# Optimization experiments

Hardware: AMD Instinct MI355X
Metric: run time of the kernel (lower is better)

## Reference

```python
import jax, jax.numpy as jnp
import numpy as np

N_NODES = 50000
N_EDGES = 800000
IN_DIM = 768
HIDDEN = 256
N_CLASSES = 10
N_GRAPHS = 128


def setup_inputs() -> dict:
    key = jax.random.key(0)
    ks = jax.random.split(key, 10)
    emb = jax.random.normal(ks[0], (N_NODES, IN_DIM), dtype=jnp.float32)
    edge_index = jax.random.randint(ks[1], (2, N_EDGES), 0, N_NODES, dtype=jnp.int32)
    batch = jnp.sort(jax.random.randint(ks[2], (N_NODES,), 0, N_GRAPHS, dtype=jnp.int32))
    # GCNConv weights (glorot-ish scale) and biases
    W1 = jax.random.normal(ks[3], (IN_DIM, HIDDEN), dtype=jnp.float32) / np.sqrt(IN_DIM)
    b1 = jnp.zeros((HIDDEN,), dtype=jnp.float32)
    W2 = jax.random.normal(ks[4], (HIDDEN, HIDDEN), dtype=jnp.float32) / np.sqrt(HIDDEN)
    b2 = jnp.zeros((HIDDEN,), dtype=jnp.float32)
    Wfc = jax.random.normal(ks[5], (HIDDEN, N_CLASSES), dtype=jnp.float32) / np.sqrt(HIDDEN)
    bfc = jnp.zeros((N_CLASSES,), dtype=jnp.float32)
    return {"emb": emb, "edge_index": edge_index, "batch": batch,
            "W1": W1, "b1": b1, "W2": W2, "b2": b2, "Wfc": Wfc, "bfc": bfc}


def _gcn_conv(x, src, dst, W, b, n_nodes):
    # PyG GCNConv: x' = D^{-1/2} (A + I) D^{-1/2} X W + b, self-loops included
    h = x @ W                                   # [N, H] dense GEMM
    deg = jax.ops.segment_sum(jnp.ones_like(dst, dtype=h.dtype), dst,
                              num_segments=n_nodes)
    dinv = jnp.where(deg > 0, jax.lax.rsqrt(deg), 0.0)
    norm = dinv[src] * dinv[dst]                # [E+N]
    msgs = h[src] * norm[:, None]               # gather [E+N, H]
    out = jax.ops.segment_sum(msgs, dst, num_segments=n_nodes)  # scatter-add
    return out + b


def reference(emb, edge_index, batch, W1, b1, W2, b2, Wfc, bfc):
    n_nodes = emb.shape[0]
    loops = jnp.arange(n_nodes, dtype=edge_index.dtype)
    src = jnp.concatenate([edge_index[0], loops])  # add self-loops
    dst = jnp.concatenate([edge_index[1], loops])

    x = jax.nn.relu(_gcn_conv(emb, src, dst, W1, b1, n_nodes))
    # F.dropout(p=0.3) is a no-op in eval mode (training=False)
    x = _gcn_conv(x, src, dst, W2, b2, n_nodes)

    # global_mean_pool over graph ids
    sums = jax.ops.segment_sum(x, batch, num_segments=N_GRAPHS)
    cnts = jax.ops.segment_sum(jnp.ones((n_nodes,), dtype=x.dtype), batch,
                               num_segments=N_GRAPHS)
    pooled = sums / jnp.maximum(cnts, 1.0)[:, None]  # [G, H]
    return pooled @ Wfc + bfc                        # [G, C]
```

## Files before the change

### kernel.cpp

```cpp
#include <hip/hip_runtime.h>

#define N_NODES 50000
#define N_EDGES 800000
#define IN_DIM 768
#define HIDDEN 256
#define N_CLASSES 10
#define N_GRAPHS 128

typedef __attribute__((ext_vector_type(8))) short bf16x8;
typedef __attribute__((ext_vector_type(4))) float f32x4;
typedef __attribute__((ext_vector_type(8))) unsigned short u16x8;

__device__ __forceinline__ float bf2f(unsigned short u) {
    union { unsigned int i; float f; } c; c.i = ((unsigned int)u) << 16; return c.f;
}
__device__ __forceinline__ unsigned short f2bf(float f) {
    unsigned int x = __float_as_uint(f);
    return (unsigned short)((x + 0x7fffu + ((x >> 16) & 1u)) >> 16);
}

__device__ __forceinline__ void gload16(const void* g, void* l) {
    __builtin_amdgcn_global_load_lds((const __attribute__((address_space(1))) void*)g,
                                     (__attribute__((address_space(3))) void*)l, 16, 0, 0);
}

__global__ void zero_int(int* p, int n) {
    int i = blockIdx.x * blockDim.x + threadIdx.x;
    if (i < n) p[i] = 0;
}

__global__ void zero_f32(float* p, int n) {
    int i = blockIdx.x * blockDim.x + threadIdx.x;
    if (i < n) p[i] = 0.f;
}

__global__ void hist_dst(const int* __restrict__ dst, int* __restrict__ cnt) {
    int e = blockIdx.x * blockDim.x + threadIdx.x;
    if (e < N_EDGES) atomicAdd(&cnt[dst[e]], 1);
}

__global__ __launch_bounds__(1024) void scan_kernel(const int* __restrict__ cnt,
                                                    int* __restrict__ rowstart,
                                                    int* __restrict__ cursor,
                                                    float* __restrict__ dinv) {
    __shared__ int wsum[16];
    __shared__ int chunk_carry;
    const int tid = threadIdx.x, lane = tid & 63, wid = tid >> 6;
    if (tid == 0) chunk_carry = 0;
    __syncthreads();
    for (int base = 0; base < N_NODES; base += 1024) {
        int i = base + tid;
        int v = (i < N_NODES) ? cnt[i] : 0;
        if (i < N_NODES) dinv[i] = rsqrtf(1.0f + (float)v);
        int s = v;
#pragma unroll
        for (int d = 1; d < 64; d <<= 1) { int t = __shfl_up(s, d); if (lane >= d) s += t; }
        if (lane == 63) wsum[wid] = s;
        __syncthreads();
        if (tid < 16) {
            int ww = wsum[tid];
#pragma unroll
            for (int d = 1; d < 16; d <<= 1) { int t = __shfl_up(ww, d); if (tid >= d) ww += t; }
            wsum[tid] = ww;
        }
        __syncthreads();
        int wpre = (wid == 0) ? 0 : wsum[wid - 1];
        int excl = chunk_carry + wpre + s - v;
        if (i < N_NODES) { rowstart[i] = excl; cursor[i] = excl; }
        int total = wsum[15];
        __syncthreads();
        if (tid == 0) chunk_carry += total;
        __syncthreads();
    }
    if (threadIdx.x == 0) rowstart[N_NODES] = chunk_carry;
}

__global__ void scatter_edges(const int* __restrict__ src, const int* __restrict__ dst,
                              int* __restrict__ cursor, int* __restrict__ col) {
    int e = blockIdx.x * blockDim.x + threadIdx.x;
    if (e >= N_EDGES) return;
    int d = dst[e];
    int pos = atomicAdd(&cursor[d], 1);
    col[pos] = src[e];
}

__global__ __launch_bounds__(256) void transpose_w_bf16(const float* __restrict__ W,
                                                        unsigned short* __restrict__ WT, int K) {
    __shared__ float t[32][33];
    int tx = threadIdx.x & 31, ty = threadIdx.x >> 5;
    int k0 = blockIdx.x * 32, n0 = blockIdx.y * 32;
#pragma unroll
    for (int i = 0; i < 4; ++i) {
        int k = k0 + ty + i * 8;
        t[ty + i * 8][tx] = W[(size_t)k * 256 + n0 + tx];
    }
    __syncthreads();
#pragma unroll
    for (int i = 0; i < 4; ++i) {
        int n = n0 + ty + i * 8;
        WT[(size_t)n * K + k0 + tx] = f2bf(t[tx][ty + i * 8]);
    }
}

template <int K, bool CVT>
__global__ __launch_bounds__(256, 4) void gemm_mfma(const void* __restrict__ Av,
                                                    const unsigned short* __restrict__ BT,
                                                    unsigned short* __restrict__ C, int M) {
    __shared__ uint4 sm[2304];
    uint4* As = sm;
    uint4* Bs = sm + 256;
    const int tid = threadIdx.x;
    const int lane = tid & 63, w = tid >> 6;
    const int lr = lane & 15, kg = lane >> 4;
    const int bm = blockIdx.x * 32;

    f32x4 acc[2][4] = {};

    for (int k0 = 0; k0 < K; k0 += 64) {
        if constexpr (CVT) {
            const float* Af = (const float*)Av;
            int r = tid >> 3, g = tid & 7;
            int gs = g ^ (r & 7);
            int rg = bm + r; rg = rg < M ? rg : M - 1;
            const float* p = &Af[(size_t)rg * K + k0 + gs * 8];
            float4 u = *(const float4*)p;
            float4 v = *(const float4*)(p + 4);
            u16x8 o;
            o[0] = f2bf(u.x); o[1] = f2bf(u.y); o[2] = f2bf(u.z); o[3] = f2bf(u.w);
            o[4] = f2bf(v.x); o[5] = f2bf(v.y); o[6] = f2bf(v.z); o[7] = f2bf(v.w);
            *(u16x8*)&As[r * 8 + g] = o;
        } else {
            const unsigned short* Ab = (const unsigned short*)Av;
            int glin = w * 64 + lane;
            int r = glin >> 3, g = glin & 7;
            int gs = g ^ (r & 7);
            int rg = bm + r; rg = rg < M ? rg : M - 1;
            gload16(&Ab[(size_t)rg * K + k0 + gs * 8], &As[w * 64]);
        }
#pragma unroll
        for (int i = 0; i < 8; ++i) {
            int glin = w * 512 + i * 64 + lane;
            int n = glin >> 3, g = glin & 7;
            int gs = g ^ (n & 7);
            gload16(&BT[(size_t)n * K + k0 + gs * 8], &Bs[w * 512 + i * 64]);
        }
        __syncthreads();

#pragma unroll
        for (int h = 0; h < 2; ++h) {
            int r0 = lr, r1 = 16 + lr;
            bf16x8 a0 = *(const bf16x8*)&As[r0 * 8 + ((4 * h + kg) ^ (r0 & 7))];
            bf16x8 a1 = *(const bf16x8*)&As[r1 * 8 + ((4 * h + kg) ^ (r1 & 7))];
#pragma unroll
            for (int f = 0; f < 4; ++f) {
                int nr = 64 * w + 16 * f + lr;
                bf16x8 bf = *(const bf16x8*)&Bs[nr * 8 + ((4 * h + kg) ^ (nr & 7))];
                acc[0][f] = __builtin_amdgcn_mfma_f32_16x16x32_bf16(bf, a0, acc[0][f], 0, 0, 0);
                acc[1][f] = __builtin_amdgcn_mfma_f32_16x16x32_bf16(bf, a1, acc[1][f], 0, 0, 0);
            }
        }
        __syncthreads();
    }
#pragma unroll
    for (int m = 0; m < 2; ++m) {
        int orow = bm + 16 * m + lr;
        if (orow < M) {
#pragma unroll
            for (int f = 0; f < 4; ++f) {
                ushort4 o = make_ushort4(f2bf(acc[m][f][0]), f2bf(acc[m][f][1]),
                                         f2bf(acc[m][f][2]), f2bf(acc[m][f][3]));
                *(ushort4*)&C[(size_t)orow * 256 + 64 * w + 16 * f + 4 * kg] = o;
            }
        }
    }
}

template <bool RELU, bool OUTBF>
__global__ __launch_bounds__(256) void agg_csr(const unsigned short* __restrict__ h,
                                               const float* __restrict__ dinv,
                                               const int* __restrict__ rowstart,
                                               const int* __restrict__ col,
                                               const float* __restrict__ bias,
                                               void* __restrict__ outv) {
    int node = (blockIdx.x * 256 + threadIdx.x) >> 6;
    if (node >= N_NODES) return;
    const int lane = threadIdx.x & 63;
    const int half = lane >> 5, sl = lane & 31;

    float dd = dinv[node];
    float acc[8] = {};

    {
        u16x8 hv = *(const u16x8*)&h[(size_t)node * 256 + sl * 8];
        float wgt = half ? 0.f : dd * dd;
#pragma unroll
        for (int i = 0; i < 8; ++i) acc[i] += bf2f(hv[i]) * wgt;
    }

    int j0 = rowstart[node], jend = rowstart[node + 1];
    for (int j = j0; j < jend; j += 2) {
        int sidx = j + half;
        bool p = sidx < jend;
        int s = p ? col[sidx] : node;
        float nrm = p ? dinv[s] * dd : 0.f;
        u16x8 v = *(const u16x8*)&h[(size_t)s * 256 + sl * 8];
#pragma unroll
        for (int i = 0; i < 8; ++i) acc[i] += bf2f(v[i]) * nrm;
    }

#pragma unroll
    for (int i = 0; i < 8; ++i) acc[i] += __shfl_xor(acc[i], 32);

    if (half == 0) {
        float4 b0 = *(const float4*)&bias[sl * 8];
        float4 b1 = *(const float4*)&bias[sl * 8 + 4];
        acc[0] += b0.x; acc[1] += b0.y; acc[2] += b0.z; acc[3] += b0.w;
        acc[4] += b1.x; acc[5] += b1.y; acc[6] += b1.z; acc[7] += b1.w;
        if (RELU) {
#pragma unroll
            for (int i = 0; i < 8; ++i) acc[i] = fmaxf(acc[i], 0.f);
        }
        if (OUTBF) {
            u16x8 o;
#pragma unroll
            for (int i = 0; i < 8; ++i) o[i] = f2bf(acc[i]);
            *(u16x8*)((unsigned short*)outv + (size_t)node * 256 + sl * 8) = o;
        } else {
            float* ob = (float*)outv + (size_t)node * 256 + sl * 8;
            *(float4*)ob = make_float4(acc[0], acc[1], acc[2], acc[3]);
            *(float4*)(ob + 4) = make_float4(acc[4], acc[5], acc[6], acc[7]);
        }
    }
}

#define POOL_CHUNK 49
__global__ __launch_bounds__(256) void pool_partial(const float* __restrict__ x,
                                                    const int* __restrict__ batch,
                                                    float* __restrict__ gsum) {
    int lo = blockIdx.x * POOL_CHUNK;
    if (lo >= N_NODES) return;
    int hi = lo + POOL_CHUNK; if (hi > N_NODES) hi = N_NODES;
    int c = threadIdx.x;
    int g = batch[lo];
    float acc = 0.f;
    for (int n = lo; n < hi; ++n) {
        int gn = batch[n];
        if (gn != g) { atomicAdd(&gsum[g * 256 + c], acc); acc = 0.f; g = gn; }
        acc += x[(size_t)n * 256 + c];
    }
    atomicAdd(&gsum[g * 256 + c], acc);
}

__global__ __launch_bounds__(256) void fc_head(const float* __restrict__ gsum,
                                               const int* __restrict__ batch,
                                               const float* __restrict__ Wfc,
                                               const float* __restrict__ bfc,
                                               float* __restrict__ out) {
    int g = blockIdx.x;
    int c = threadIdx.x;
    int lo = 0, hi = N_NODES;
    while (lo < hi) { int m = (lo + hi) >> 1; if (batch[m] < g) lo = m + 1; else hi = m; }
    int lo2 = lo, hi2 = N_NODES;
    while (lo2 < hi2) { int m = (lo2 + hi2) >> 1; if (batch[m] < g + 1) lo2 = m + 1; else hi2 = m; }
    float inv = 1.0f / fmaxf((float)(lo2 - lo), 1.0f);
    __shared__ float pooled[256];
    pooled[c] = gsum[(size_t)g * 256 + c] * inv;
    __syncthreads();
    if (c < N_CLASSES) {
        float acc = bfc[c];
        for (int k = 0; k < 256; ++k) acc += pooled[k] * Wfc[k * N_CLASSES + c];
        out[g * N_CLASSES + c] = acc;
    }
}

extern "C" void kernel_launch(void* const* d_in, const int* in_sizes, int n_in,
                              void* d_out, int out_size, void* d_ws, size_t ws_size,
                              hipStream_t stream) {
    const float* emb  = (const float*)d_in[0];
    const int*   eidx = (const int*)d_in[1];
    const int*   batch= (const int*)d_in[2];
    const float* W1   = (const float*)d_in[3];
    const float* b1   = (const float*)d_in[4];
    const float* W2   = (const float*)d_in[5];
    const float* b2   = (const float*)d_in[6];
    const float* Wfc  = (const float*)d_in[7];
    const float* bfc  = (const float*)d_in[8];
    float* out = (float*)d_out;

    const int* src = eidx;
    const int* dst = eidx + N_EDGES;

    char* ws = (char*)d_ws;
    size_t off = 0;
    auto alloc = [&](size_t bytes) { void* p = ws + off; off += (bytes + 1023) & ~(size_t)1023; return p; };
    int*   rowcnt   = (int*)alloc(N_NODES * 4);
    int*   rowstart = (int*)alloc((N_NODES + 1) * 4);
    int*   cursor   = (int*)alloc(N_NODES * 4);
    int*   col      = (int*)alloc(N_EDGES * 4);
    float* dinv     = (float*)alloc(N_NODES * 4);
    float* gsum     = (float*)alloc((size_t)N_GRAPHS * 256 * 4);
    unsigned short* W1T = (unsigned short*)alloc((size_t)HIDDEN * IN_DIM * 2);
    unsigned short* W2T = (unsigned short*)alloc((size_t)HIDDEN * HIDDEN * 2);
    unsigned short* bufH = (unsigned short*)alloc((size_t)N_NODES * 256 * 2);
    unsigned short* x1 = (unsigned short*)alloc((size_t)N_NODES * 256 * 2);
    float* x2 = (float*)alloc((size_t)N_NODES * 256 * 4);

    const int NB = (N_NODES + 255) / 256;
    const int EBk = (N_EDGES + 255) / 256;
    const int AGG_B = (N_NODES * 64 + 255) / 256;
    dim3 gemm_grid((N_NODES + 31) / 32, 1);
    const int POOL_B = (N_NODES + POOL_CHUNK - 1) / POOL_CHUNK;

    zero_int<<<NB, 256, 0, stream>>>(rowcnt, N_NODES);
    hist_dst<<<EBk, 256, 0, stream>>>(dst, rowcnt);
    scan_kernel<<<1, 1024, 0, stream>>>(rowcnt, rowstart, cursor, dinv);
    scatter_edges<<<EBk, 256, 0, stream>>>(src, dst, cursor, col);
    zero_f32<<<(N_GRAPHS * 256 + 255) / 256, 256, 0, stream>>>(gsum, N_GRAPHS * 256);

    transpose_w_bf16<<<dim3(IN_DIM / 32, 8), 256, 0, stream>>>(W1, W1T, IN_DIM);
    transpose_w_bf16<<<dim3(HIDDEN / 32, 8), 256, 0, stream>>>(W2, W2T, HIDDEN);

    gemm_mfma<IN_DIM, true><<<gemm_grid, 256, 0, stream>>>(emb, W1T, bufH, N_NODES);
    agg_csr<true, true><<<AGG_B, 256, 0, stream>>>(bufH, dinv, rowstart, col, b1, x1);

    gemm_mfma<HIDDEN, false><<<gemm_grid, 256, 0, stream>>>(x1, W2T, bufH, N_NODES);
    agg_csr<false, false><<<AGG_B, 256, 0, stream>>>(bufH, dinv, rowstart, col, b2, x2);

    pool_partial<<<POOL_B, 256, 0, stream>>>(x2, batch, gsum);
    fc_head<<<N_GRAPHS, 256, 0, stream>>>(gsum, batch, Wfc, bfc, out);
}
```

Baseline: 431.8 us.

## Stage full A row-tile in LDS once and read B fragments directly from global

The GEMM now loads the block's entire 32xK A tile into LDS up front, with a single barrier and an XOR swizzle, replacing the per-K-step A and B staging with two barriers per step. B fragments are read straight from global memory (expected to hit L2/L1, since the weights are small and shared across blocks) instead of being staged through LDS via global_load_lds. This removes the sync overhead and the LDS traffic for B. In exchange it uses much more LDS for K=768 (48KB), which may lower occupancy, and loses the overlap of loads with compute.

```diff
diff --git a/kernel.cpp b/kernel.cpp
--- a/kernel.cpp
+++ b/kernel.cpp
@@ -17,11 +17,6 @@
 __device__ __forceinline__ unsigned short f2bf(float f) {
     unsigned int x = __float_as_uint(f);
     return (unsigned short)((x + 0x7fffu + ((x >> 16) & 1u)) >> 16);
-}
-
-__device__ __forceinline__ void gload16(const void* g, void* l) {
-    __builtin_amdgcn_global_load_lds((const __attribute__((address_space(1))) void*)g,
-                                     (__attribute__((address_space(3))) void*)l, 16, 0, 0);
 }
 
 __global__ void zero_int(int* p, int n) {
@@ -106,61 +101,63 @@
 __global__ __launch_bounds__(256, 4) void gemm_mfma(const void* __restrict__ Av,
                                                     const unsigned short* __restrict__ BT,
                                                     unsigned short* __restrict__ C, int M) {
-    __shared__ uint4 sm[2304];
-    uint4* As = sm;
-    uint4* Bs = sm + 256;
+    constexpr int NG = K / 8;
+    __shared__ uint4 As[32 * NG];
     const int tid = threadIdx.x;
     const int lane = tid & 63, w = tid >> 6;
     const int lr = lane & 15, kg = lane >> 4;
     const int bm = blockIdx.x * 32;
 
-    f32x4 acc[2][4] = {};
-
-    for (int k0 = 0; k0 < K; k0 += 64) {
-        if constexpr (CVT) {
-            const float* Af = (const float*)Av;
-            int r = tid >> 3, g = tid & 7;
-            int gs = g ^ (r & 7);
+    if constexpr (CVT) {
+        const float* Af = (const float*)Av;
+#pragma unroll
+        for (int i = 0; i < (32 * NG) / 256; ++i) {
+            int glin = i * 256 + tid;
+            int r = glin / NG, c = glin % NG;
             int rg = bm + r; rg = rg < M ? rg : M - 1;
-            const float* p = &Af[(size_t)rg * K + k0 + gs * 8];
+            const float* p = &Af[(size_t)rg * K + c * 8];
             float4 u = *(const float4*)p;
             float4 v = *(const float4*)(p + 4);
             u16x8 o;
             o[0] = f2bf(u.x); o[1] = f2bf(u.y); o[2] = f2bf(u.z); o[3] = f2bf(u.w);
             o[4] = f2bf(v.x); o[5] = f2bf(v.y); o[6] = f2bf(v.z); o[7] = f2bf(v.w);
-            *(u16x8*)&As[r * 8 + g] = o;
-        } else {
-            const unsigned short* Ab = (const unsigned short*)Av;
-            int glin = w * 64 + lane;
-            int r = glin >> 3, g = glin & 7;
-            int gs = g ^ (r & 7);
+            int csw = (c & ~7) | ((c & 7) ^ (r & 7));
+            *(u16x8*)&As[r * NG + csw] = o;
+        }
+    } else {
+        const unsigned short* Ab = (const unsigned short*)Av;
+#pragma unroll
+        for (int i = 0; i < (32 * NG) / 256; ++i) {
+            int glin = i * 256 + tid;
+            int r = glin / NG, c = glin % NG;
             int rg = bm + r; rg = rg < M ? rg : M - 1;
-            gload16(&Ab[(size_t)rg * K + k0 + gs * 8], &As[w * 64]);
-        }
-#pragma unroll
-        for (int i = 0; i < 8; ++i) {
-            int glin = w * 512 + i * 64 + lane;
-            int n = glin >> 3, g = glin & 7;
-            int gs = g ^ (n & 7);
-            gload16(&BT[(size_t)n * K + k0 + gs * 8], &Bs[w * 512 + i * 64]);
-        }
-        __syncthreads();
-
+            uint4 v = *(const uint4*)&Ab[(size_t)rg * K + c * 8];
+            int csw = (c & ~7) | ((c & 7) ^ (r & 7));
+            As[r * NG + csw] = v;
+        }
+    }
+    __syncthreads();
+
+    f32x4 acc[2][4] = {};
+    const int r0 = lr, r1 = 16 + lr;
+    const unsigned short* Brow0 = &BT[(size_t)(64 * w + lr) * K];
+
+    for (int g0 = 0; g0 < NG; g0 += 8) {
 #pragma unroll
         for (int h = 0; h < 2; ++h) {
-            int r0 = lr, r1 = 16 + lr;
-            bf16x8 a0 = *(const bf16x8*)&As[r0 * 8 + ((4 * h + kg) ^ (r0 & 7))];
-            bf16x8 a1 = *(const bf16x8*)&As[r1 * 8 + ((4 * h + kg) ^ (r1 & 7))];
+            int gc = 4 * h + kg;
+            bf16x8 a0 = *(const bf16x8*)&As[r0 * NG + g0 + (gc ^ (r0 & 7))];
+            bf16x8 a1 = *(const bf16x8*)&As[r1 * NG + g0 + (gc ^ (r1 & 7))];
+            int koff = (g0 + gc) * 8;
 #pragma unroll
             for (int f = 0; f < 4; ++f) {
-                int nr = 64 * w + 16 * f + lr;
-                bf16x8 bf = *(const bf16x8*)&Bs[nr * 8 + ((4 * h + kg) ^ (nr & 7))];
+                bf16x8 bf = *(const bf16x8*)&Brow0[(size_t)(16 * f) * K + koff];
                 acc[0][f] = __builtin_amdgcn_mfma_f32_16x16x32_bf16(bf, a0, acc[0][f], 0, 0, 0);
                 acc[1][f] = __builtin_amdgcn_mfma_f32_16x16x32_bf16(bf, a1, acc[1][f], 0, 0, 0);
             }
         }
-        __syncthreads();
-    }
+    }
+
 #pragma unroll
     for (int m = 0; m < 2; ++m) {
         int orow = bm + 16 * m + lr;
```

Result: slower. 490.8 us (+13.6%).
